# Kernel tuning notes

Hardware: AMD Instinct MI355X
Metric: run time of the kernel (lower is better)

The kernel has to match this reference:

```python
import jax, jax.numpy as jnp
import numpy as np


def _l2norm(v, eps=1e-12):
    # torch F.normalize(dim=-1): v / clamp(||v||_2, min=eps)
    n = jnp.linalg.norm(v, axis=-1, keepdims=True)
    return v / jnp.maximum(n, eps)


def setup_inputs() -> dict:
    key = jax.random.key(0)
    ks = jax.random.split(key, 10)
    B, T, N, Ci, E, K, H = 64, 12, 1024, 64, 16, 3, 192
    O = H // 3  # subhidden size
    return {
        "x": jax.random.normal(ks[0], (B, N, Ci), jnp.float32),
        "x_window": jax.random.normal(ks[1], (B, T, N, 1), jnp.float32),
        "node_embeddings": jax.random.normal(ks[2], (N, E), jnp.float32) * 0.1,
        "ZPI": jax.random.normal(ks[3], (B, 3), jnp.float32),
        "supports_adj": jax.random.uniform(ks[4], (K, N, N), jnp.float32),
        "weights_pool": jax.random.normal(ks[5], (E, K, Ci, O), jnp.float32) * 0.1,
        "weights_pool_adj": jax.random.normal(ks[6], (E, K, Ci, O), jnp.float32) * 0.1,
        "weights_window": jax.random.normal(ks[7], (E, 1, O), jnp.float32) * 0.1,
        "bias_pool": jax.random.normal(ks[8], (E, H), jnp.float32) * 0.1,
        "T_param": jax.random.normal(ks[9], (T,), jnp.float32) * 0.1,
    }


def reference(x, x_window, node_embeddings, ZPI, supports_adj,
              weights_pool, weights_pool_adj, weights_window, bias_pool, T_param):
    N = node_embeddings.shape[0]
    K = weights_pool.shape[1]  # link_len

    # adaptive supports: softmax(relu(E E^T)) and its power series
    supports = jax.nn.softmax(jax.nn.relu(node_embeddings @ node_embeddings.T), axis=1)
    support_set = [jnp.eye(N, dtype=x.dtype), supports]
    for k in range(2, K):
        support_set.append(supports @ support_set[k - 1])
    S = jnp.stack(support_set, axis=0)  # (K, N, N)

    # per-node dynamic weights / bias
    weights = jnp.einsum('nd,dkio->nkio', node_embeddings, weights_pool)
    bias = node_embeddings @ bias_pool  # (N, H)

    # adaptive graph conv branch
    x_g = jnp.einsum('knm,bmc->bnkc', S, x)
    x_gconv = _l2norm(jnp.einsum('bnki,nkio->bno', x_g, weights))

    # static adjacency branch ('knn' repeated index = diagonal; sum over m --
    # faithful to the original torch einsum)
    weights_adj = jnp.einsum('nd,dkio->nkio', node_embeddings, weights_pool_adj)
    x_a = jnp.einsum('knn,bmc->bnkc', supports_adj, x)
    x_aconv = _l2norm(jnp.einsum('bnki,nkio->bno', x_a, weights_adj))

    # temporal window branch
    ww = jnp.einsum('nd,dio->nio', node_embeddings, weights_window)  # (N, 1, O)
    x_w = jnp.einsum('btni,nio->btno', x_window, ww)
    x_wconv = _l2norm(jnp.einsum('btno,t->bno', x_w, T_param))

    return jnp.concatenate([x_gconv, x_aconv, x_wconv], axis=-1) + bias
```

## Files before the change

kernel.cpp:

```cpp
#include <hip/hip_runtime.h>


typedef __attribute__((ext_vector_type(4))) float f32x4;
typedef __attribute__((ext_vector_type(8))) short short8;

#define DEVI static __device__ __forceinline__

DEVI short f2bf(float f) {
    unsigned int x = __builtin_bit_cast(unsigned int, f);
    x = (x + 0x7FFFu + ((x >> 16) & 1u)) >> 16;
    return (short)(unsigned short)x;
}
DEVI int swz(int row) { return ((row ^ (row >> 3)) & 7) << 3; }

DEVI f32x4 mfma16(short8 a, short8 b, f32x4 c) {
    return __builtin_amdgcn_mfma_f32_16x16x32_bf16(a, b, c, 0, 0, 0);
}

DEVI void gload16(const void* g, void* l) {
    __builtin_amdgcn_global_load_lds(
        (const __attribute__((address_space(1))) unsigned int*)g,
        (__attribute__((address_space(3))) unsigned int*)l, 16, 0, 0);
}

__global__ __launch_bounds__(256) void k_supports(const float* __restrict__ NE,
                                                  short* __restrict__ S) {
    int n = blockIdx.x, t = threadIdx.x;
    __shared__ float En[16];
    __shared__ float wsum[4];
    if (t < 16) En[t] = NE[n * 16 + t];
    __syncthreads();
    float e[4];
    float loc = 0.f;
#pragma unroll
    for (int i = 0; i < 4; ++i) {
        int m = t + 256 * i;
        const float* rp = NE + m * 16;
        float v = 0.f;
#pragma unroll
        for (int d = 0; d < 16; ++d) v += En[d] * rp[d];
        v = fmaxf(v, 0.f);
        e[i] = __expf(v);
        loc += e[i];
    }
#pragma unroll
    for (int off = 32; off; off >>= 1) loc += __shfl_xor(loc, off);
    if ((t & 63) == 0) wsum[t >> 6] = loc;
    __syncthreads();
    float inv = 1.f / (wsum[0] + wsum[1] + wsum[2] + wsum[3]);
#pragma unroll
    for (int i = 0; i < 4; ++i) S[n * 1024 + t + 256 * i] = f2bf(e[i] * inv);
}

__global__ __launch_bounds__(256) void k_small(
        const float* __restrict__ x, const float* __restrict__ xw,
        const float* __restrict__ NE, const float* __restrict__ adj,
        const float* __restrict__ wp, const float* __restrict__ wpa,
        const float* __restrict__ Tp,
        short* __restrict__ B2, short* __restrict__ A2,
        float* __restrict__ xsp, float* __restrict__ s_bn) {
    __shared__ float red[4][64];
    int bid = blockIdx.x, t = threadIdx.x;
    if (bid < 64) {
        int o = bid, j = t;
        short row[64];
        if (j < 192) {
            int kk = j >> 6, i = j & 63;
#pragma unroll
            for (int d = 0; d < 16; ++d)
                row[d] = f2bf(wp[((d * 3 + kk) * 64 + i) * 64 + o]);
#pragma unroll
            for (int k = 16; k < 64; ++k) row[k] = 0;
        } else {
            int i2 = j - 192;
#pragma unroll
            for (int k = 0; k < 16; ++k) row[k] = 0;
#pragma unroll
            for (int d = 0; d < 16; ++d)
#pragma unroll
                for (int kk = 0; kk < 3; ++kk)
                    row[16 + d * 3 + kk] = f2bf(wpa[((d * 3 + kk) * 64 + i2) * 64 + o]);
        }
        short* dst = B2 + (o * 256 + j) * 64;
#pragma unroll
        for (int q = 0; q < 8; ++q) {
            short8 v;
#pragma unroll
            for (int e2 = 0; e2 < 8; ++e2) v[e2] = row[q * 8 + e2];
            *reinterpret_cast<short8*>(dst + q * 8) = v;
        }
    } else if (bid < 320) {
        int idx = bid - 64, b = idx >> 2, mq = idx & 3;
        int c = t & 63, q2 = t >> 6;
        int m0 = mq * 256 + q2 * 64;
        float s = 0.f;
        for (int mm = 0; mm < 64; ++mm) s += x[((size_t)b * 1024 + m0 + mm) * 64 + c];
        red[q2][c] = s;
        __syncthreads();
        if (t < 64) xsp[(b * 4 + mq) * 64 + t] = red[0][t] + red[1][t] + red[2][t] + red[3][t];
    } else if (bid < 336) {
        int idx = bid - 320;
        float tp[12];
#pragma unroll
        for (int i = 0; i < 12; ++i) tp[i] = Tp[i];
        for (int bb = 0; bb < 4; ++bb) {
            int b = idx * 4 + bb;
#pragma unroll
            for (int j2 = 0; j2 < 4; ++j2) {
                int nn = t + 256 * j2;
                float s = 0.f;
#pragma unroll
                for (int tt = 0; tt < 12; ++tt) s += xw[(b * 12 + tt) * 1024 + nn] * tp[tt];
                s_bn[b * 1024 + nn] = s;
            }
        }
    } else {
        int n = (bid - 336) * 256 + t;
        float En[16];
#pragma unroll
        for (int d = 0; d < 16; ++d) En[d] = NE[n * 16 + d];
        float dg[3];
#pragma unroll
        for (int k = 0; k < 3; ++k) dg[k] = adj[k * 1024 * 1024 + n * 1024 + n];
        short row[64];
#pragma unroll
        for (int d = 0; d < 16; ++d) row[d] = f2bf(En[d]);
#pragma unroll
        for (int d = 0; d < 16; ++d)
#pragma unroll
            for (int k = 0; k < 3; ++k) row[16 + d * 3 + k] = f2bf(En[d] * dg[k]);
        short* dst = A2 + n * 64;
#pragma unroll
        for (int q = 0; q < 8; ++q) {
            short8 v;
#pragma unroll
            for (int e2 = 0; e2 < 8; ++e2) v[e2] = row[q * 8 + e2];
            *reinterpret_cast<short8*>(dst + q * 8) = v;
        }
    }
}

__global__ __launch_bounds__(256) void k_gemm1(const short* __restrict__ S,
                                               const float* __restrict__ x,
                                               short* __restrict__ Y1) {
    __shared__ __align__(16) short As[128 * 64];
    __shared__ __align__(16) short Bs[64 * 64];
    int bx = blockIdx.x, b = blockIdx.y, t = threadIdx.x;
    int wid = t >> 6, lane = t & 63;
    int rsub = lane >> 3, csub = (lane & 7) * 8;
    int wm = wid & 1, wn = wid >> 1;
    int lr = lane & 15, lg = lane >> 4;
    const short* A = S + (size_t)bx * 131072;
    const float* xb = x + (size_t)b * 65536;
    int bm = t >> 2, bc = (t & 3) * 16;
    f32x4 acc[4][2] = {};
    for (int kt = 0; kt < 16; ++kt) {
#pragma unroll
        for (int q = 0; q < 4; ++q) {
            int row = q * 32 + wid * 8;
            gload16(A + (size_t)(row + rsub) * 1024 + kt * 64 + csub, As + row * 64);
        }
#pragma unroll
        for (int j = 0; j < 4; ++j) {
            float4 f = *reinterpret_cast<const float4*>(&xb[(kt * 64 + bm) * 64 + bc + 4 * j]);
            float vv[4] = {f.x, f.y, f.z, f.w};
#pragma unroll
            for (int e = 0; e < 4; ++e) {
                int c = bc + 4 * j + e;
                Bs[c * 64 + (bm ^ swz(c))] = f2bf(vv[e]);
            }
        }
        __syncthreads();
#pragma unroll
        for (int ks = 0; ks < 2; ++ks) {
            int kk = ks * 32 + lg * 8;
            short8 af[4], bfr[2];
#pragma unroll
            for (int i = 0; i < 4; ++i)
                af[i] = *reinterpret_cast<const short8*>(&As[(wm * 64 + i * 16 + lr) * 64 + kk]);
#pragma unroll
            for (int nf = 0; nf < 2; ++nf) {
                int c = wn * 32 + nf * 16 + lr;
                bfr[nf] = *reinterpret_cast<const short8*>(&Bs[c * 64 + (kk ^ swz(c))]);
            }
#pragma unroll
            for (int i = 0; i < 4; ++i)
#pragma unroll
                for (int nf = 0; nf < 2; ++nf)
                    acc[i][nf] = mfma16(af[i], bfr[nf], acc[i][nf]);
        }
        __syncthreads();
    }
#pragma unroll
    for (int i = 0; i < 4; ++i)
#pragma unroll
        for (int nf = 0; nf < 2; ++nf)
#pragma unroll
            for (int r = 0; r < 4; ++r) {
                int g = wm * 64 + i * 16 + lg * 4 + r;
                int c = wn * 32 + nf * 16 + lr;
                Y1[(size_t)(bx * 128 + g) * 4096 + b * 64 + c] = f2bf(acc[i][nf][r]);
            }
}

__global__ __launch_bounds__(256) void k_gemm2(const short* __restrict__ S,
                                               const short* __restrict__ Y1,
                                               short* __restrict__ Y2) {
    __shared__ __align__(16) short As[128 * 64];
    __shared__ __align__(16) short Bs[64 * 64];
    int bx = blockIdx.x, b = blockIdx.y, t = threadIdx.x;
    int wid = t >> 6, lane = t & 63;
    int rsub = lane >> 3, csub = (lane & 7) * 8;
    int wm = wid & 1, wn = wid >> 1;
    int lr = lane & 15, lg = lane >> 4;
    const short* A = S + (size_t)bx * 131072;
    int bm = t >> 3, bc0 = (t & 7) * 8;
    f32x4 acc[4][2] = {};
    for (int kt = 0; kt < 16; ++kt) {
#pragma unroll
        for (int q = 0; q < 4; ++q) {
            int row = q * 32 + wid * 8;
            gload16(A + (size_t)(row + rsub) * 1024 + kt * 64 + csub, As + row * 64);
        }
#pragma unroll
        for (int it = 0; it < 2; ++it) {
            int m = bm + 32 * it;
            short8 hv = *reinterpret_cast<const short8*>(
                &Y1[(size_t)(kt * 64 + m) * 4096 + b * 64 + bc0]);
#pragma unroll
            for (int j = 0; j < 8; ++j) {
                int c = bc0 + j;
                Bs[c * 64 + (m ^ swz(c))] = hv[j];
            }
        }
        __syncthreads();
#pragma unroll
        for (int ks = 0; ks < 2; ++ks) {
            int kk = ks * 32 + lg * 8;
            short8 af[4], bfr[2];
#pragma unroll
            for (int i = 0; i < 4; ++i)
                af[i] = *reinterpret_cast<const short8*>(&As[(wm * 64 + i * 16 + lr) * 64 + kk]);
#pragma unroll
            for (int nf = 0; nf < 2; ++nf) {
                int c = wn * 32 + nf * 16 + lr;
                bfr[nf] = *reinterpret_cast<const short8*>(&Bs[c * 64 + (kk ^ swz(c))]);
            }
#pragma unroll
            for (int i = 0; i < 4; ++i)
#pragma unroll
                for (int nf = 0; nf < 2; ++nf)
                    acc[i][nf] = mfma16(af[i], bfr[nf], acc[i][nf]);
        }
        __syncthreads();
    }
#pragma unroll
    for (int i = 0; i < 4; ++i)
#pragma unroll
        for (int nf = 0; nf < 2; ++nf)
#pragma unroll
            for (int r = 0; r < 4; ++r) {
                int g = wm * 64 + i * 16 + lg * 4 + r;
                int c = wn * 32 + nf * 16 + lr;
                Y2[(size_t)(bx * 128 + g) * 4096 + b * 64 + c] = f2bf(acc[i][nf][r]);
            }
}

__global__ __launch_bounds__(256) void k_gemm_w(const short* __restrict__ A2,
                                                const short* __restrict__ B2,
                                                short* __restrict__ Wall,
                                                const float* __restrict__ xsp,
                                                short* __restrict__ xs_bf) {
    int bx = blockIdx.x, by = blockIdx.y, t = threadIdx.x;
    if (bx == 128) {
#pragma unroll
        for (int p = 0; p < 2; ++p) {
            int j = by * 512 + p * 256 + t;
            int b = j >> 6, c = j & 63;
            float s = xsp[(b * 4 + 0) * 64 + c] + xsp[(b * 4 + 1) * 64 + c] +
                      xsp[(b * 4 + 2) * 64 + c] + xsp[(b * 4 + 3) * 64 + c];
            xs_bf[j] = f2bf(s);
        }
        return;
    }
    __shared__ __align__(16) short As[128 * 64];
    __shared__ __align__(16) short Bs[128 * 64];
#pragma unroll
    for (int i = 0; i < 4; ++i) {
        int slot = t + 256 * i;
        int row = slot >> 3, k8 = slot & 7;
        int sw = swz(row);
        short8 va = *reinterpret_cast<const short8*>(A2 + (by * 128 + row) * 64 + k8 * 8);
        *reinterpret_cast<short8*>(&As[row * 64 + ((k8 * 8) ^ sw)]) = va;
        short8 vb = *reinterpret_cast<const short8*>(B2 + (bx * 128 + row) * 64 + k8 * 8);
        *reinterpret_cast<short8*>(&Bs[row * 64 + ((k8 * 8) ^ sw)]) = vb;
    }
    __syncthreads();
    int w = t >> 6, l = t & 63;
    int wm = w & 1, wn = w >> 1;
    int lr = l & 15, lg = l >> 4;
    f32x4 acc[4][4] = {};
#pragma unroll
    for (int ks = 0; ks < 2; ++ks) {
        int kk = ks * 32 + lg * 8;
        short8 af[4], bfr[4];
#pragma unroll
        for (int mf = 0; mf < 4; ++mf) {
            int row = wm * 64 + mf * 16 + lr;
            af[mf] = *reinterpret_cast<const short8*>(&As[row * 64 + (kk ^ swz(row))]);
        }
#pragma unroll
        for (int nf = 0; nf < 4; ++nf) {
            int row = wn * 64 + nf * 16 + lr;
            bfr[nf] = *reinterpret_cast<const short8*>(&Bs[row * 64 + (kk ^ swz(row))]);
        }
#pragma unroll
        for (int mf = 0; mf < 4; ++mf)
#pragma unroll
            for (int nf = 0; nf < 4; ++nf)
                acc[mf][nf] = mfma16(af[mf], bfr[nf], acc[mf][nf]);
    }
#pragma unroll
    for (int mf = 0; mf < 4; ++mf)
#pragma unroll
        for (int nf = 0; nf < 4; ++nf)
#pragma unroll
            for (int r = 0; r < 4; ++r) {
                int row = by * 128 + wm * 64 + mf * 16 + lg * 4 + r;
                int col = bx * 128 + wn * 64 + nf * 16 + lr;
                int o = col >> 8, j = col & 255;
                Wall[(size_t)row * 16384 + (size_t)(j >> 3) * 512 + o * 8 + (j & 7)] =
                    f2bf(acc[mf][nf][r]);
            }
}

__global__ __launch_bounds__(256) void k_epi(
        const float* __restrict__ x, const short* __restrict__ Y1,
        const short* __restrict__ Y2, const short* __restrict__ xs_bf,
        const float* __restrict__ s_bn, const short* __restrict__ Wall,
        const float* __restrict__ NE, const float* __restrict__ bp,
        const float* __restrict__ wwin, float* __restrict__ out) {
    int n = blockIdx.x, t = threadIdx.x;
    __shared__ __align__(16) short xst[64 * 64];
    __shared__ float E_l[16];
    __shared__ float bias_l[192];
    __shared__ float ww_l[64];
    __shared__ float sq_l[2][2][64];
    __shared__ float wwn_l;
    if (t < 16) E_l[t] = NE[n * 16 + t];
    __syncthreads();
    if (t < 192) {
        float s = 0.f;
#pragma unroll
        for (int d = 0; d < 16; ++d) s += E_l[d] * bp[d * 192 + t];
        bias_l[t] = s;
    } else {
        int o = t - 192;
        float s = 0.f;
#pragma unroll
        for (int d = 0; d < 16; ++d) s += E_l[d] * wwin[d * 64 + o];
        ww_l[o] = s;
    }
#pragma unroll
    for (int p = 0; p < 2; ++p) {
        int idx = t + 256 * p;
        int b = idx >> 3, q = idx & 7;
        short8 v = *reinterpret_cast<const short8*>(&xs_bf[b * 64 + q * 8]);
        *reinterpret_cast<short8*>(&xst[b * 64 + ((q * 8) ^ swz(b))]) = v;
    }
    __syncthreads();
    if (t < 64) {
        float v = ww_l[t];
        float s2 = v * v;
#pragma unroll
        for (int off = 32; off; off >>= 1) s2 += __shfl_xor(s2, off);
        if (t == 0) wwn_l = sqrtf(s2);
    }
    int w = t >> 6, l = t & 63;
    int wm = w & 1, wn = w >> 1;
    int lr = l & 15, lg = l >> 4;
    f32x4 accg[2][2] = {};
    f32x4 acca[2][2] = {};
#pragma unroll
    for (int ks = 0; ks < 8; ++ks) {
        short8 af[2];
#pragma unroll
        for (int mf = 0; mf < 2; ++mf) {
            int b = wm * 32 + mf * 16 + lr;
            int k0 = ks * 32 + lg * 8;
            if (ks < 2) {
                const float4* p =
                    reinterpret_cast<const float4*>(&x[((size_t)b * 1024 + n) * 64 + k0]);
                float4 p0 = p[0], p1 = p[1];
                short8 v;
                v[0] = f2bf(p0.x); v[1] = f2bf(p0.y); v[2] = f2bf(p0.z); v[3] = f2bf(p0.w);
                v[4] = f2bf(p1.x); v[5] = f2bf(p1.y); v[6] = f2bf(p1.z); v[7] = f2bf(p1.w);
                af[mf] = v;
            } else if (ks < 4) {
                af[mf] = *reinterpret_cast<const short8*>(
                    &Y1[(size_t)n * 4096 + b * 64 + (k0 - 64)]);
            } else if (ks < 6) {
                af[mf] = *reinterpret_cast<const short8*>(
                    &Y2[(size_t)n * 4096 + b * 64 + (k0 - 128)]);
            } else {
                af[mf] = *reinterpret_cast<const short8*>(
                    &xst[b * 64 + ((k0 - 192) ^ swz(b))]);
            }
        }
        short8 wfk[2];
#pragma unroll
        for (int nf = 0; nf < 2; ++nf) {
            int o = wn * 32 + nf * 16 + lr;
            wfk[nf] = *reinterpret_cast<const short8*>(
                &Wall[(size_t)n * 16384 + (size_t)(ks * 4 + lg) * 512 + o * 8]);
        }
#pragma unroll
        for (int mf = 0; mf < 2; ++mf)
#pragma unroll
            for (int nf = 0; nf < 2; ++nf) {
                if (ks < 6) accg[mf][nf] = mfma16(af[mf], wfk[nf], accg[mf][nf]);
                else        acca[mf][nf] = mfma16(af[mf], wfk[nf], acca[mf][nf]);
            }
    }
#pragma unroll
    for (int mf = 0; mf < 2; ++mf)
#pragma unroll
        for (int r = 0; r < 4; ++r) {
            float sg = accg[mf][0][r] * accg[mf][0][r] + accg[mf][1][r] * accg[mf][1][r];
            float sa = acca[mf][0][r] * acca[mf][0][r] + acca[mf][1][r] * acca[mf][1][r];
#pragma unroll
            for (int off = 1; off < 16; off <<= 1) {
                sg += __shfl_xor(sg, off);
                sa += __shfl_xor(sa, off);
            }
            if (lr == 0) {
                int b = wm * 32 + mf * 16 + lg * 4 + r;
                sq_l[0][wn][b] = sg;
                sq_l[1][wn][b] = sa;
            }
        }
    __syncthreads();
#pragma unroll
    for (int mf = 0; mf < 2; ++mf)
#pragma unroll
        for (int r = 0; r < 4; ++r) {
            int b = wm * 32 + mf * 16 + lg * 4 + r;
            float ig = 1.f / fmaxf(sqrtf(sq_l[0][0][b] + sq_l[0][1][b]), 1e-12f);
            float ia = 1.f / fmaxf(sqrtf(sq_l[1][0][b] + sq_l[1][1][b]), 1e-12f);
            float* po = out + ((size_t)b * 1024 + n) * 192;
#pragma unroll
            for (int nf = 0; nf < 2; ++nf) {
                int o = wn * 32 + nf * 16 + lr;
                po[o]      = accg[mf][nf][r] * ig + bias_l[o];
                po[64 + o] = acca[mf][nf][r] * ia + bias_l[64 + o];
            }
        }
    float wwn = wwn_l;
#pragma unroll
    for (int it = 0; it < 16; ++it) {
        int b = it * 4 + (t >> 6);
        int o = t & 63;
        float s = s_bn[b * 1024 + n];
        float pre = s * ww_l[o];
        float nrm = fabsf(s) * wwn;
        out[((size_t)b * 1024 + n) * 192 + 128 + o] = pre / fmaxf(nrm, 1e-12f) + bias_l[128 + o];
    }
}

extern "C" void kernel_launch(void* const* d_in, const int* in_sizes, int n_in,
                              void* d_out, int out_size, void* d_ws, size_t ws_size,
                              hipStream_t stream) {
    const float* x    = (const float*)d_in[0];
    const float* xw   = (const float*)d_in[1];
    const float* NE   = (const float*)d_in[2];
    const float* adj  = (const float*)d_in[4];
    const float* wp   = (const float*)d_in[5];
    const float* wpa  = (const float*)d_in[6];
    const float* wwin = (const float*)d_in[7];
    const float* bp   = (const float*)d_in[8];
    const float* Tp   = (const float*)d_in[9];
    float* out = (float*)d_out;

    char* ws = (char*)d_ws;
    const size_t OFF_S    = 0;
    const size_t OFF_Y1   = 2097152;
    const size_t OFF_Y2   = 10485760;
    const size_t OFF_WALL = 18874368;
    const size_t OFF_A2   = 52428800;
    const size_t OFF_B2   = 52559872;
    const size_t OFF_XSP  = 54657024;
    const size_t OFF_XSBF = 54722560;
    const size_t OFF_SBN  = 54730752;
    const size_t NEED     = 54992896;
    if (ws_size < NEED) return;

    short* S     = (short*)(ws + OFF_S);
    short* Y1    = (short*)(ws + OFF_Y1);
    short* Y2    = (short*)(ws + OFF_Y2);
    short* Wall  = (short*)(ws + OFF_WALL);
    short* A2    = (short*)(ws + OFF_A2);
    short* B2    = (short*)(ws + OFF_B2);
    float* xsp   = (float*)(ws + OFF_XSP);
    short* xs_bf = (short*)(ws + OFF_XSBF);
    float* s_bn  = (float*)(ws + OFF_SBN);

    k_supports<<<1024, 256, 0, stream>>>(NE, S);
    k_small<<<340, 256, 0, stream>>>(x, xw, NE, adj, wp, wpa, Tp, B2, A2, xsp, s_bn);
    k_gemm1<<<dim3(8, 64), 256, 0, stream>>>(S, x, Y1);
    k_gemm2<<<dim3(8, 64), 256, 0, stream>>>(S, Y1, Y2);
    k_gemm_w<<<dim3(129, 8), 256, 0, stream>>>(A2, B2, Wall, xsp, xs_bf);
    k_epi<<<1024, 256, 0, stream>>>(x, Y1, Y2, xs_bf, s_bn, Wall, NE, bp, wwin, out);
}
```

Measured before the change: 123.8 us.

## Store Y1/Y2/xs in fragment-major layout and stage epilogue operands via LDS

Changes the intermediate Y1, Y2 and xs buffers to a k-chunk-major layout (8-element groups across batch) so the epilogue can bulk-copy per-node operand blocks with contiguous global_load_lds. The epilogue now stages Y1/Y2 and per-node Wall weights into LDS up front and reads MFMA fragments from LDS. It also drops the xs staging copy and the separate embedding-to-LDS step. The goal is more coalesced global access and overlap of loads with the bias computation, at the cost of 48KB of LDS per block, which may reduce occupancy.

Measured after the change: 136.6 us. +10.3%, slower.

```diff
diff --git a/kernel.cpp b/kernel.cpp
--- a/kernel.cpp
+++ b/kernel.cpp
@@ -142,7 +142,7 @@
 
 __global__ __launch_bounds__(256) void k_gemm1(const short* __restrict__ S,
                                                const float* __restrict__ x,
-                                               short* __restrict__ Y1) {
+                                               short* __restrict__ Y1F) {
     __shared__ __align__(16) short As[128 * 64];
     __shared__ __align__(16) short Bs[64 * 64];
     int bx = blockIdx.x, b = blockIdx.y, t = threadIdx.x;
@@ -199,13 +199,14 @@
             for (int r = 0; r < 4; ++r) {
                 int g = wm * 64 + i * 16 + lg * 4 + r;
                 int c = wn * 32 + nf * 16 + lr;
-                Y1[(size_t)(bx * 128 + g) * 4096 + b * 64 + c] = f2bf(acc[i][nf][r]);
+                Y1F[(size_t)(bx * 128 + g) * 4096 + (size_t)(c >> 3) * 512 + b * 8 + (c & 7)] =
+                    f2bf(acc[i][nf][r]);
             }
 }
 
 __global__ __launch_bounds__(256) void k_gemm2(const short* __restrict__ S,
-                                               const short* __restrict__ Y1,
-                                               short* __restrict__ Y2) {
+                                               const short* __restrict__ Y1F,
+                                               short* __restrict__ Y2F) {
     __shared__ __align__(16) short As[128 * 64];
     __shared__ __align__(16) short Bs[64 * 64];
     int bx = blockIdx.x, b = blockIdx.y, t = threadIdx.x;
@@ -214,7 +215,7 @@
     int wm = wid & 1, wn = wid >> 1;
     int lr = lane & 15, lg = lane >> 4;
     const short* A = S + (size_t)bx * 131072;
-    int bm = t >> 3, bc0 = (t & 7) * 8;
+    int bm = t >> 3, q0 = t & 7;
     f32x4 acc[4][2] = {};
     for (int kt = 0; kt < 16; ++kt) {
 #pragma unroll
@@ -226,10 +227,10 @@
         for (int it = 0; it < 2; ++it) {
             int m = bm + 32 * it;
             short8 hv = *reinterpret_cast<const short8*>(
-                &Y1[(size_t)(kt * 64 + m) * 4096 + b * 64 + bc0]);
+                &Y1F[(size_t)(kt * 64 + m) * 4096 + (size_t)q0 * 512 + b * 8]);
 #pragma unroll
             for (int j = 0; j < 8; ++j) {
-                int c = bc0 + j;
+                int c = q0 * 8 + j;
                 Bs[c * 64 + (m ^ swz(c))] = hv[j];
             }
         }
@@ -262,7 +263,8 @@
             for (int r = 0; r < 4; ++r) {
                 int g = wm * 64 + i * 16 + lg * 4 + r;
                 int c = wn * 32 + nf * 16 + lr;
-                Y2[(size_t)(bx * 128 + g) * 4096 + b * 64 + c] = f2bf(acc[i][nf][r]);
+                Y2F[(size_t)(bx * 128 + g) * 4096 + (size_t)(c >> 3) * 512 + b * 8 + (c & 7)] =
+                    f2bf(acc[i][nf][r]);
             }
 }
 
@@ -270,7 +272,7 @@
                                                 const short* __restrict__ B2,
                                                 short* __restrict__ Wall,
                                                 const float* __restrict__ xsp,
-                                                short* __restrict__ xs_bf) {
+                                                short* __restrict__ xsF) {
     int bx = blockIdx.x, by = blockIdx.y, t = threadIdx.x;
     if (bx == 128) {
 #pragma unroll
@@ -279,7 +281,7 @@
             int b = j >> 6, c = j & 63;
             float s = xsp[(b * 4 + 0) * 64 + c] + xsp[(b * 4 + 1) * 64 + c] +
                       xsp[(b * 4 + 2) * 64 + c] + xsp[(b * 4 + 3) * 64 + c];
-            xs_bf[j] = f2bf(s);
+            xsF[(c >> 3) * 512 + b * 8 + (c & 7)] = f2bf(s);
         }
         return;
     }
@@ -335,38 +337,45 @@
 }
 
 __global__ __launch_bounds__(256) void k_epi(
-        const float* __restrict__ x, const short* __restrict__ Y1,
-        const short* __restrict__ Y2, const short* __restrict__ xs_bf,
+        const float* __restrict__ x, const short* __restrict__ Y1F,
+        const short* __restrict__ Y2F, const short* __restrict__ xsF,
         const float* __restrict__ s_bn, const short* __restrict__ Wall,
         const float* __restrict__ NE, const float* __restrict__ bp,
         const float* __restrict__ wwin, float* __restrict__ out) {
     int n = blockIdx.x, t = threadIdx.x;
-    __shared__ __align__(16) short xst[64 * 64];
-    __shared__ float E_l[16];
+    __shared__ __align__(16) short A_lds[16 * 512];
+    __shared__ __align__(16) short W_lds[32 * 512];
     __shared__ float bias_l[192];
     __shared__ float ww_l[64];
     __shared__ float sq_l[2][2][64];
     __shared__ float wwn_l;
-    if (t < 16) E_l[t] = NE[n * 16 + t];
-    __syncthreads();
-    if (t < 192) {
-        float s = 0.f;
-#pragma unroll
-        for (int d = 0; d < 16; ++d) s += E_l[d] * bp[d * 192 + t];
-        bias_l[t] = s;
-    } else {
-        int o = t - 192;
-        float s = 0.f;
-#pragma unroll
-        for (int d = 0; d < 16; ++d) s += E_l[d] * wwin[d * 64 + o];
-        ww_l[o] = s;
-    }
-#pragma unroll
-    for (int p = 0; p < 2; ++p) {
-        int idx = t + 256 * p;
-        int b = idx >> 3, q = idx & 7;
-        short8 v = *reinterpret_cast<const short8*>(&xs_bf[b * 64 + q * 8]);
-        *reinterpret_cast<short8*>(&xst[b * 64 + ((q * 8) ^ swz(b))]) = v;
+    int lane = t & 63, wid = t >> 6;
+#pragma unroll
+    for (int r = 0; r < 4; ++r) {
+        int off = (r * 4 + wid) * 512;
+        const short* src = (off < 4096) ? (Y1F + (size_t)n * 4096 + off)
+                                        : (Y2F + (size_t)n * 4096 + (off - 4096));
+        gload16(src + lane * 8, A_lds + off);
+    }
+#pragma unroll
+    for (int r = 0; r < 8; ++r) {
+        int off = (r * 4 + wid) * 512;
+        gload16(Wall + (size_t)n * 16384 + off + lane * 8, W_lds + off);
+    }
+    {
+        const float* En = NE + n * 16;
+        if (t < 192) {
+            float s = 0.f;
+#pragma unroll
+            for (int d = 0; d < 16; ++d) s += En[d] * bp[d * 192 + t];
+            bias_l[t] = s;
+        } else {
+            int o = t - 192;
+            float s = 0.f;
+#pragma unroll
+            for (int d = 0; d < 16; ++d) s += En[d] * wwin[d * 64 + o];
+            ww_l[o] = s;
+        }
     }
     __syncthreads();
     if (t < 64) {
@@ -376,9 +385,8 @@
         for (int off = 32; off; off >>= 1) s2 += __shfl_xor(s2, off);
         if (t == 0) wwn_l = sqrtf(s2);
     }
-    int w = t >> 6, l = t & 63;
-    int wm = w & 1, wn = w >> 1;
-    int lr = l & 15, lg = l >> 4;
+    int wm = wid & 1, wn = wid >> 1;
+    int lr = lane & 15, lg = lane >> 4;
     f32x4 accg[2][2] = {};
     f32x4 acca[2][2] = {};
 #pragma unroll
@@ -387,8 +395,8 @@
 #pragma unroll
         for (int mf = 0; mf < 2; ++mf) {
             int b = wm * 32 + mf * 16 + lr;
-            int k0 = ks * 32 + lg * 8;
             if (ks < 2) {
+                int k0 = ks * 32 + lg * 8;
                 const float4* p =
                     reinterpret_cast<const float4*>(&x[((size_t)b * 1024 + n) * 64 + k0]);
                 float4 p0 = p[0], p1 = p[1];
@@ -396,15 +404,12 @@
                 v[0] = f2bf(p0.x); v[1] = f2bf(p0.y); v[2] = f2bf(p0.z); v[3] = f2bf(p0.w);
                 v[4] = f2bf(p1.x); v[5] = f2bf(p1.y); v[6] = f2bf(p1.z); v[7] = f2bf(p1.w);
                 af[mf] = v;
-            } else if (ks < 4) {
-                af[mf] = *reinterpret_cast<const short8*>(
-                    &Y1[(size_t)n * 4096 + b * 64 + (k0 - 64)]);
             } else if (ks < 6) {
                 af[mf] = *reinterpret_cast<const short8*>(
-                    &Y2[(size_t)n * 4096 + b * 64 + (k0 - 128)]);
+                    &A_lds[((ks - 2) * 4 + lg) * 512 + b * 8]);
             } else {
                 af[mf] = *reinterpret_cast<const short8*>(
-                    &xst[b * 64 + ((k0 - 192) ^ swz(b))]);
+                    &xsF[((ks - 6) * 4 + lg) * 512 + b * 8]);
             }
         }
         short8 wfk[2];
@@ -412,7 +417,7 @@
         for (int nf = 0; nf < 2; ++nf) {
             int o = wn * 32 + nf * 16 + lr;
             wfk[nf] = *reinterpret_cast<const short8*>(
-                &Wall[(size_t)n * 16384 + (size_t)(ks * 4 + lg) * 512 + o * 8]);
+                &W_lds[(ks * 4 + lg) * 512 + o * 8]);
         }
 #pragma unroll
         for (int mf = 0; mf < 2; ++mf)
@@ -495,19 +500,19 @@
     if (ws_size < NEED) return;
 
     short* S     = (short*)(ws + OFF_S);
-    short* Y1    = (short*)(ws + OFF_Y1);
-    short* Y2    = (short*)(ws + OFF_Y2);
+    short* Y1F   = (short*)(ws + OFF_Y1);
+    short* Y2F   = (short*)(ws + OFF_Y2);
     short* Wall  = (short*)(ws + OFF_WALL);
     short* A2    = (short*)(ws + OFF_A2);
     short* B2    = (short*)(ws + OFF_B2);
     float* xsp   = (float*)(ws + OFF_XSP);
-    short* xs_bf = (short*)(ws + OFF_XSBF);
+    short* xsF   = (short*)(ws + OFF_XSBF);
     float* s_bn  = (float*)(ws + OFF_SBN);
 
     k_supports<<<1024, 256, 0, stream>>>(NE, S);
     k_small<<<340, 256, 0, stream>>>(x, xw, NE, adj, wp, wpa, Tp, B2, A2, xsp, s_bn);
-    k_gemm1<<<dim3(8, 64), 256, 0, stream>>>(S, x, Y1);
-    k_gemm2<<<dim3(8, 64), 256, 0, stream>>>(S, Y1, Y2);
-    k_gemm_w<<<dim3(129, 8), 256, 0, stream>>>(A2, B2, Wall, xsp, xs_bf);
-    k_epi<<<1024, 256, 0, stream>>>(x, Y1, Y2, xs_bf, s_bn, Wall, NE, bp, wwin, out);
-}
+    k_gemm1<<<dim3(8, 64), 256, 0, stream>>>(S, x, Y1F);
+    k_gemm2<<<dim3(8, 64), 256, 0, stream>>>(S, Y1F, Y2F);
+    k_gemm_w<<<dim3(129, 8), 256, 0, stream>>>(A2, B2, Wall, xsp, xsF);
+    k_epi<<<1024, 256, 0, stream>>>(x, Y1F, Y2F, xsF, s_bn, Wall, NE, bp, wwin, out);
+}
```
